# Kernel optimization log

Measured on AMD Instinct MI355X. Metric: run time of the kernel, lower is better.

Reference implementation:

```python
import jax, jax.numpy as jnp
import numpy as np

B, T, D, A = 16, 2048, 512, 64


def setup_inputs() -> dict:
    key = jax.random.key(0)
    ks = jax.random.split(key, 7)
    s = 1.0 / np.sqrt(D)
    return {
        "inp": jax.random.normal(ks[0], (B, T, D), dtype=jnp.float32),
        "Wq": jax.random.normal(ks[1], (D, A), dtype=jnp.float32) * s,
        "bq": jax.random.normal(ks[2], (A,), dtype=jnp.float32) * 0.01,
        "Wk": jax.random.normal(ks[3], (D, A), dtype=jnp.float32) * s,
        "bk": jax.random.normal(ks[4], (A,), dtype=jnp.float32) * 0.01,
        "Wv": jax.random.normal(ks[5], (D, A), dtype=jnp.float32) * s,
        "bv": jax.random.normal(ks[6], (A,), dtype=jnp.float32) * 0.01,
    }


def reference(inp, Wq, bq, Wk, bk, Wv, bv):
    # Projections: (B,T,D) @ (D,A) -> (B,T,A)
    Q = inp @ Wq + bq
    K = inp @ Wk + bk
    V = inp @ Wv + bv
    # Scaled QK^T: (B,T,T)
    scores = jnp.einsum("btd,bsd->bts", Q, K) / jnp.sqrt(jnp.float32(A))
    # Sign-based K padding mask: mask[b, s] = sign(|sum_a K[b,s,a]|)
    k_mask = jnp.sign(jnp.abs(K.sum(axis=-1)))  # (B,T)
    scores = jnp.where(k_mask[:, None, :] == 0, jnp.float32(1e-8), scores)
    att = jax.nn.softmax(scores, axis=-1)
    # Sign-based Q mask broadcast along the key axis (faithful to Mask module)
    q_mask = jnp.sign(jnp.abs(Q.sum(axis=-1)))  # (B,T)
    att = att * q_mask[:, None, :]
    # dropout_keep_prob == 1 -> dropout is identity
    ctx = jnp.einsum("bts,bsa->bta", att, V)  # (B,T,A)
    # inp^T @ ctx -> (B,D,A), then sum over A -> (B,D)
    out = jnp.einsum("btd,bta->bd", inp, ctx)
    return out
```

## Files before the change

kernel.cpp:

```cpp
#include <hip/hip_runtime.h>

#define B_ 16
#define T_ 2048
#define D_ 512
#define SCALE_LOG2E 0.18033688f

typedef __bf16 bf16x8 __attribute__((ext_vector_type(8)));
typedef float  f32x4  __attribute__((ext_vector_type(4)));

__device__ inline unsigned short f2bf(float f){
    union { float f; unsigned u; } x; x.f = f;
    unsigned r = x.u + 0x7fffu + ((x.u >> 16) & 1u);
    return (unsigned short)(r >> 16);
}

__device__ inline bf16x8 ldfrag(const unsigned short* p){
    uint4 v = *reinterpret_cast<const uint4*>(p);
    return __builtin_bit_cast(bf16x8, v);
}


__global__ void setup_kernel(const float* __restrict__ Wq, const float* __restrict__ Wk,
                             const float* __restrict__ Wv, const float* __restrict__ bq,
                             const float* __restrict__ bk, const float* __restrict__ bv,
                             unsigned short* __restrict__ WcT, float* __restrict__ bsum,
                             float* __restrict__ out)
{
    int e = blockIdx.x * 256 + threadIdx.x;
    if (e < 73728){
        int j = e >> 9, d = e & 511;
        float v;
        if (j < 64)       v = Wq[d * 64 + j];
        else if (j < 128) v = Wk[d * 64 + (j - 64)];
        else if (j < 131){
            const float* src = (j == 128) ? Wq : (j == 129) ? Wk : Wv;
            const float4* p = reinterpret_cast<const float4*>(&src[d * 64]);
            v = 0.f;
            #pragma unroll
            for (int i = 0; i < 16; i++){ float4 t = p[i]; v += (t.x + t.y) + (t.z + t.w); }
        }
        else v = 0.f;
        WcT[j * 512 + d] = f2bf(v);
    } else if (e < 73744){
        int mm = e - 73728;
        float s = 0.f;
        const float* src = (mm == 0) ? bq : (mm == 1) ? bk : bv;
        if (mm < 3){
            const float4* p = reinterpret_cast<const float4*>(src);
            #pragma unroll
            for (int i = 0; i < 16; i++){ float4 t = p[i]; s += (t.x + t.y) + (t.z + t.w); }
        }
        bsum[mm] = s;
    } else if (e < 81936){
        out[e - 73744] = 0.f;
    }
}

__global__ __launch_bounds__(256) void proj_kernel(
    const float* __restrict__ inp, const unsigned short* __restrict__ WcT,
    const float* __restrict__ bq, const float* __restrict__ bk,
    const float* __restrict__ bsum,
    unsigned short* __restrict__ Qb, unsigned short* __restrict__ Kb,
    float* __restrict__ wvp)
{
    __shared__ __align__(16) unsigned short Af[2][4 * 512];
    __shared__ __align__(16) unsigned short Bf[2][9 * 512];
    __shared__ float kzsh[64];
    const int tid  = threadIdx.x;
    const int r0   = blockIdx.x * 64;
    const int lane = tid & 63, wvid = tid >> 6;
    const int m = lane & 15, q = lane >> 4;
    const int mh = wvid >> 1, nh = wvid & 1;

    const int ar = tid >> 2, aseg = tid & 3;
    const int a_off = (ar >> 4) * 512 + (aseg * 16 + (ar & 15)) * 8;
    const float* a_src = &inp[(size_t)(r0 + ar) * 512 + aseg * 8];
    const unsigned short* b_src0 = &WcT[(((tid      ) >> 6) * 16 + (tid & 15)) * 512 + ((tid >> 4) & 3) * 8];
    const unsigned short* b_src1 = &WcT[(((tid + 256) >> 6) * 16 + (tid & 15)) * 512 + ((tid >> 4) & 3) * 8];
    const unsigned short* b_src2 = &WcT[(((tid + 512) >> 6) * 16 + (tid & 15)) * 512 + ((tid >> 4) & 3) * 8];
    const int b_off0 = tid * 8, b_off1 = (tid + 256) * 8, b_off2 = (tid + 512) * 8;

    f32x4 acc[5][2];
    #pragma unroll
    for (int t = 0; t < 5; t++){
        acc[t][0] = (f32x4){0.f, 0.f, 0.f, 0.f};
        acc[t][1] = (f32x4){0.f, 0.f, 0.f, 0.f};
    }

    float4 ga0 = *reinterpret_cast<const float4*>(a_src);
    float4 ga1 = *reinterpret_cast<const float4*>(a_src + 4);
    uint4 gb0 = *reinterpret_cast<const uint4*>(b_src0);
    uint4 gb1 = *reinterpret_cast<const uint4*>(b_src1);
    uint4 gb2 = (tid < 64) ? *reinterpret_cast<const uint4*>(b_src2) : (uint4){0,0,0,0};

    const int ntile = 5 - nh;
    const int tbase = nh * 5;

    for (int it = 0; it < 16; it++){
        const int p = it & 1;
        unsigned short* Ab = Af[p];
        unsigned short* Bb = Bf[p];
        uint4 pk;
        pk.x = f2bf(ga0.x) | ((unsigned)f2bf(ga0.y) << 16);
        pk.y = f2bf(ga0.z) | ((unsigned)f2bf(ga0.w) << 16);
        pk.z = f2bf(ga1.x) | ((unsigned)f2bf(ga1.y) << 16);
        pk.w = f2bf(ga1.z) | ((unsigned)f2bf(ga1.w) << 16);
        *reinterpret_cast<uint4*>(&Ab[a_off]) = pk;
        *reinterpret_cast<uint4*>(&Bb[b_off0]) = gb0;
        *reinterpret_cast<uint4*>(&Bb[b_off1]) = gb1;
        if (tid < 64) *reinterpret_cast<uint4*>(&Bb[b_off2]) = gb2;
        __syncthreads();
        if (it < 15){
            const int kn = (it + 1) * 32;
            ga0 = *reinterpret_cast<const float4*>(a_src + kn);
            ga1 = *reinterpret_cast<const float4*>(a_src + kn + 4);
            gb0 = *reinterpret_cast<const uint4*>(b_src0 + kn);
            gb1 = *reinterpret_cast<const uint4*>(b_src1 + kn);
            if (tid < 64) gb2 = *reinterpret_cast<const uint4*>(b_src2 + kn);
        }
        bf16x8 a0 = ldfrag(&Ab[(mh * 2    ) * 512 + lane * 8]);
        bf16x8 a1 = ldfrag(&Ab[(mh * 2 + 1) * 512 + lane * 8]);
        #pragma unroll
        for (int t = 0; t < 5; t++){
            if (t < ntile){
                bf16x8 bfr = ldfrag(&Bb[(tbase + t) * 512 + lane * 8]);
                acc[t][0] = __builtin_amdgcn_mfma_f32_16x16x32_bf16(a0, bfr, acc[t][0], 0, 0, 0);
                acc[t][1] = __builtin_amdgcn_mfma_f32_16x16x32_bf16(a1, bfr, acc[t][1], 0, 0, 0);
            }
        }
    }
    __syncthreads();

    if (nh == 1){
        const float bs = bsum[m];
        #pragma unroll
        for (int f = 0; f < 2; f++){
            #pragma unroll
            for (int i = 0; i < 4; i++){
                int rl = mh * 32 + f * 16 + q * 4 + i;
                float val = acc[3][f][i] + bs;
                float qsv = __shfl(val, (lane & 48));
                float ksv = __shfl(val, (lane & 48) | 1);
                float vsv = __shfl(val, (lane & 48) | 2);
                if (m == 0){
                    kzsh[rl] = (ksv == 0.f) ? 0.f : 1.f;
                    wvp[(size_t)r0 + rl] = (qsv == 0.f) ? 0.f : vsv;
                }
            }
        }
    }
    __syncthreads();

    if (nh == 0){
        float bqv[4];
        #pragma unroll
        for (int t = 0; t < 4; t++) bqv[t] = bq[t * 16 + m];
        const float bkv0 = bk[m];
        #pragma unroll
        for (int f = 0; f < 2; f++){
            #pragma unroll
            for (int i = 0; i < 4; i++){
                int rl = mh * 32 + f * 16 + q * 4 + i;
                size_t r = (size_t)r0 + rl;
                float kz = kzsh[rl];
                #pragma unroll
                for (int t = 0; t < 4; t++)
                    Qb[r * 64 + t * 16 + m] = f2bf((acc[t][f][i] + bqv[t]) * SCALE_LOG2E);
                Kb[r * 64 + m] = f2bf((acc[4][f][i] + bkv0) * kz);
            }
        }
    } else {
        float bkv[3];
        #pragma unroll
        for (int t = 0; t < 3; t++) bkv[t] = bk[16 + t * 16 + m];
        #pragma unroll
        for (int f = 0; f < 2; f++){
            #pragma unroll
            for (int i = 0; i < 4; i++){
                int rl = mh * 32 + f * 16 + q * 4 + i;
                size_t r = (size_t)r0 + rl;
                float kz = kzsh[rl];
                #pragma unroll
                for (int t = 0; t < 3; t++)
                    Kb[r * 64 + 16 + t * 16 + m] = f2bf((acc[t][f][i] + bkv[t]) * kz);
            }
        }
    }
}

__global__ __launch_bounds__(512) void attn_kernel(
    const unsigned short* __restrict__ Qb, const unsigned short* __restrict__ Kb,
    const float* __restrict__ wvp, float* __restrict__ num_s, float* __restrict__ den_s)
{
    __shared__ __align__(16) unsigned short Kf[2][8 * 512];
    const int tid = threadIdx.x;
    const int lane = tid & 63, wvid = tid >> 6;
    const int m = lane & 15, q = lane >> 4;
    const int b  = blockIdx.y;
    const int t0 = blockIdx.x * 256 + wvid * 32;
    const int s0 = blockIdx.z * 512;
    const size_t base = (size_t)b * T_;
    const size_t zoff = (size_t)blockIdx.z * (B_ * T_);

    const unsigned short* qp = &Qb[(base + t0 + m) * 64 + q * 8];
    bf16x8 a00 = ldfrag(qp),            a01 = ldfrag(qp + 32);
    bf16x8 a10 = ldfrag(qp + 16 * 64),  a11 = ldfrag(qp + 16 * 64 + 32);

    const unsigned short* ksrc = &Kb[(base + s0 + (wvid >> 1) * 16 + m) * 64 + (wvid & 1) * 32 + q * 8];
    const int k_off = wvid * 512 + lane * 8;
    uint4 stg = *reinterpret_cast<const uint4*>(ksrc);

    float num0[4] = {0,0,0,0}, den0[4] = {0,0,0,0};
    float num1[4] = {0,0,0,0}, den1[4] = {0,0,0,0};

    for (int it = 0; it < 8; it++){
        const int p = it & 1;
        *reinterpret_cast<uint4*>(&Kf[p][k_off]) = stg;
        __syncthreads();
        if (it < 7) stg = *reinterpret_cast<const uint4*>(ksrc + (it + 1) * 64 * 64);
        float w[4];
        #pragma unroll
        for (int st = 0; st < 4; st++) w[st] = wvp[base + s0 + it * 64 + st * 16 + m];
        #pragma unroll
        for (int st = 0; st < 4; st++){
            bf16x8 b0 = ldfrag(&Kf[p][(st * 2    ) * 512 + lane * 8]);
            bf16x8 b1 = ldfrag(&Kf[p][(st * 2 + 1) * 512 + lane * 8]);
            f32x4 z0 = (f32x4){0.f,0.f,0.f,0.f};
            z0 = __builtin_amdgcn_mfma_f32_16x16x32_bf16(a00, b0, z0, 0, 0, 0);
            z0 = __builtin_amdgcn_mfma_f32_16x16x32_bf16(a01, b1, z0, 0, 0, 0);
            f32x4 z1 = (f32x4){0.f,0.f,0.f,0.f};
            z1 = __builtin_amdgcn_mfma_f32_16x16x32_bf16(a10, b0, z1, 0, 0, 0);
            z1 = __builtin_amdgcn_mfma_f32_16x16x32_bf16(a11, b1, z1, 0, 0, 0);
            float wst = w[st];
            #pragma unroll
            for (int i = 0; i < 4; i++){
                float e0 = exp2f(z0[i]);
                den0[i] += e0; num0[i] = fmaf(e0, wst, num0[i]);
                float e1 = exp2f(z1[i]);
                den1[i] += e1; num1[i] = fmaf(e1, wst, num1[i]);
            }
        }
    }
    #pragma unroll
    for (int s = 1; s < 16; s <<= 1){
        #pragma unroll
        for (int i = 0; i < 4; i++){
            num0[i] += __shfl_xor(num0[i], s); den0[i] += __shfl_xor(den0[i], s);
            num1[i] += __shfl_xor(num1[i], s); den1[i] += __shfl_xor(den1[i], s);
        }
    }
    if (m == 0){
        #pragma unroll
        for (int i = 0; i < 4; i++){
            num_s[zoff + base + t0 + q * 4 + i]      = num0[i];
            den_s[zoff + base + t0 + q * 4 + i]      = den0[i];
            num_s[zoff + base + t0 + 16 + q * 4 + i] = num1[i];
            den_s[zoff + base + t0 + 16 + q * 4 + i] = den1[i];
        }
    }
}

__global__ __launch_bounds__(256) void out_kernel(
    const float* __restrict__ inp, const float* __restrict__ num_s,
    const float* __restrict__ den_s, float* __restrict__ out)
{
    __shared__ float csh[32];
    const int tid = threadIdx.x;
    const int b   = blockIdx.y;
    const int t0  = blockIdx.x * 32;
    const size_t base = (size_t)b * T_;
    if (tid < 32){
        size_t idx = base + t0 + tid;
        float n = num_s[idx] + num_s[32768 + idx] + num_s[65536 + idx] + num_s[98304 + idx];
        float d = den_s[idx] + den_s[32768 + idx] + den_s[65536 + idx] + den_s[98304 + idx];
        csh[tid] = n / d;
    }
    __syncthreads();
    const float2* ip = reinterpret_cast<const float2*>(inp + (base + t0) * 512);
    float a0 = 0.f, a1 = 0.f;
    #pragma unroll 8
    for (int t = 0; t < 32; t++){
        float ct = csh[t];
        float2 v = ip[(size_t)t * 256 + tid];
        a0 = fmaf(v.x, ct, a0);
        a1 = fmaf(v.y, ct, a1);
    }
    atomicAdd(&out[b * 512 + 2 * tid],     a0);
    atomicAdd(&out[b * 512 + 2 * tid + 1], a1);
}

extern "C" void kernel_launch(void* const* d_in, const int* in_sizes, int n_in,
                              void* d_out, int out_size, void* d_ws, size_t ws_size,
                              hipStream_t stream)
{
    const float* inp = (const float*)d_in[0];
    const float* Wq  = (const float*)d_in[1];
    const float* bq  = (const float*)d_in[2];
    const float* Wk  = (const float*)d_in[3];
    const float* bk  = (const float*)d_in[4];
    const float* Wv  = (const float*)d_in[5];
    const float* bv  = (const float*)d_in[6];
    float* out = (float*)d_out;

    char* ws = (char*)d_ws;
    unsigned short* WcT = (unsigned short*)(ws);
    float* bsum         = (float*)(ws + 147456);
    unsigned short* Qb  = (unsigned short*)(ws + 262144);
    unsigned short* Kb  = (unsigned short*)(ws + 4456448);
    float* wvp          = (float*)(ws + 8650752);
    float* num_s        = (float*)(ws + 8781824);
    float* den_s        = (float*)(ws + 9306112);

    setup_kernel<<<321, 256, 0, stream>>>(Wq, Wk, Wv, bq, bk, bv, WcT, bsum, out);
    proj_kernel<<<512, 256, 0, stream>>>(inp, WcT, bq, bk, bsum, Qb, Kb, wvp);
    attn_kernel<<<dim3(8, 16, 4), 512, 0, stream>>>(Qb, Kb, wvp, num_s, den_s);
    out_kernel<<<dim3(64, 16), 256, 0, stream>>>(inp, num_s, den_s, out);
}
```

Baseline: 156.7 us.

## Fuse projection, attention and output into one persistent kernel with grid barriers

```diff
diff --git a/kernel.cpp b/kernel.cpp
--- a/kernel.cpp
+++ b/kernel.cpp
@@ -3,6 +3,7 @@
 #define B_ 16
 #define T_ 2048
 #define D_ 512
+#define GRID_ 512
 #define SCALE_LOG2E 0.18033688f
 
 typedef __bf16 bf16x8 __attribute__((ext_vector_type(8)));
@@ -19,14 +20,25 @@
     return __builtin_bit_cast(bf16x8, v);
 }
 
-
-__global__ void setup_kernel(const float* __restrict__ Wq, const float* __restrict__ Wk,
-                             const float* __restrict__ Wv, const float* __restrict__ bq,
-                             const float* __restrict__ bk, const float* __restrict__ bv,
-                             unsigned short* __restrict__ WcT, float* __restrict__ bsum,
-                             float* __restrict__ out)
+__device__ inline void grid_bar(unsigned* cnt){
+    __syncthreads();
+    if (threadIdx.x == 0){
+        __hip_atomic_fetch_add(cnt, 1u, __ATOMIC_ACQ_REL, __HIP_MEMORY_SCOPE_AGENT);
+        while (__hip_atomic_load(cnt, __ATOMIC_ACQUIRE, __HIP_MEMORY_SCOPE_AGENT) < (unsigned)GRID_)
+            __builtin_amdgcn_s_sleep(1);
+    }
+    __syncthreads();
+}
+
+
+__global__ void init_kernel(const float* __restrict__ Wq, const float* __restrict__ Wk,
+                            const float* __restrict__ Wv, const float* __restrict__ bq,
+                            const float* __restrict__ bk, const float* __restrict__ bv,
+                            unsigned short* __restrict__ WcT, float* __restrict__ bsum,
+                            float* __restrict__ out, unsigned* __restrict__ bar)
 {
     int e = blockIdx.x * 256 + threadIdx.x;
+    if (e < 16) bar[e] = 0u;
     if (e < 73728){
         int j = e >> 9, d = e & 511;
         float v;
@@ -56,237 +68,250 @@
     }
 }
 
-__global__ __launch_bounds__(256) void proj_kernel(
+__global__ __launch_bounds__(256, 2) void mega_kernel(
     const float* __restrict__ inp, const unsigned short* __restrict__ WcT,
     const float* __restrict__ bq, const float* __restrict__ bk,
     const float* __restrict__ bsum,
     unsigned short* __restrict__ Qb, unsigned short* __restrict__ Kb,
-    float* __restrict__ wvp)
+    float* __restrict__ wvp, float* __restrict__ num_s, float* __restrict__ den_s,
+    float* __restrict__ out, unsigned* __restrict__ bar)
 {
-    __shared__ __align__(16) unsigned short Af[2][4 * 512];
-    __shared__ __align__(16) unsigned short Bf[2][9 * 512];
-    __shared__ float kzsh[64];
+    __shared__ union {
+        struct { __align__(16) unsigned short Af[2][2048];
+                 __align__(16) unsigned short Bf[2][4608];
+                 float kz[64]; } p;
+        struct { __align__(16) unsigned short Kf[2][4096]; } a;
+        struct { float csh[32]; } o;
+    } U;
     const int tid  = threadIdx.x;
-    const int r0   = blockIdx.x * 64;
+    const int blk  = blockIdx.x;
     const int lane = tid & 63, wvid = tid >> 6;
     const int m = lane & 15, q = lane >> 4;
-    const int mh = wvid >> 1, nh = wvid & 1;
-
-    const int ar = tid >> 2, aseg = tid & 3;
-    const int a_off = (ar >> 4) * 512 + (aseg * 16 + (ar & 15)) * 8;
-    const float* a_src = &inp[(size_t)(r0 + ar) * 512 + aseg * 8];
-    const unsigned short* b_src0 = &WcT[(((tid      ) >> 6) * 16 + (tid & 15)) * 512 + ((tid >> 4) & 3) * 8];
-    const unsigned short* b_src1 = &WcT[(((tid + 256) >> 6) * 16 + (tid & 15)) * 512 + ((tid >> 4) & 3) * 8];
-    const unsigned short* b_src2 = &WcT[(((tid + 512) >> 6) * 16 + (tid & 15)) * 512 + ((tid >> 4) & 3) * 8];
-    const int b_off0 = tid * 8, b_off1 = (tid + 256) * 8, b_off2 = (tid + 512) * 8;
-
-    f32x4 acc[5][2];
-    #pragma unroll
-    for (int t = 0; t < 5; t++){
-        acc[t][0] = (f32x4){0.f, 0.f, 0.f, 0.f};
-        acc[t][1] = (f32x4){0.f, 0.f, 0.f, 0.f};
-    }
-
-    float4 ga0 = *reinterpret_cast<const float4*>(a_src);
-    float4 ga1 = *reinterpret_cast<const float4*>(a_src + 4);
-    uint4 gb0 = *reinterpret_cast<const uint4*>(b_src0);
-    uint4 gb1 = *reinterpret_cast<const uint4*>(b_src1);
-    uint4 gb2 = (tid < 64) ? *reinterpret_cast<const uint4*>(b_src2) : (uint4){0,0,0,0};
-
-    const int ntile = 5 - nh;
-    const int tbase = nh * 5;
-
-    for (int it = 0; it < 16; it++){
-        const int p = it & 1;
-        unsigned short* Ab = Af[p];
-        unsigned short* Bb = Bf[p];
-        uint4 pk;
-        pk.x = f2bf(ga0.x) | ((unsigned)f2bf(ga0.y) << 16);
-        pk.y = f2bf(ga0.z) | ((unsigned)f2bf(ga0.w) << 16);
-        pk.z = f2bf(ga1.x) | ((unsigned)f2bf(ga1.y) << 16);
-        pk.w = f2bf(ga1.z) | ((unsigned)f2bf(ga1.w) << 16);
-        *reinterpret_cast<uint4*>(&Ab[a_off]) = pk;
-        *reinterpret_cast<uint4*>(&Bb[b_off0]) = gb0;
-        *reinterpret_cast<uint4*>(&Bb[b_off1]) = gb1;
-        if (tid < 64) *reinterpret_cast<uint4*>(&Bb[b_off2]) = gb2;
-        __syncthreads();
-        if (it < 15){
-            const int kn = (it + 1) * 32;
-            ga0 = *reinterpret_cast<const float4*>(a_src + kn);
-            ga1 = *reinterpret_cast<const float4*>(a_src + kn + 4);
-            gb0 = *reinterpret_cast<const uint4*>(b_src0 + kn);
-            gb1 = *reinterpret_cast<const uint4*>(b_src1 + kn);
-            if (tid < 64) gb2 = *reinterpret_cast<const uint4*>(b_src2 + kn);
-        }
-        bf16x8 a0 = ldfrag(&Ab[(mh * 2    ) * 512 + lane * 8]);
-        bf16x8 a1 = ldfrag(&Ab[(mh * 2 + 1) * 512 + lane * 8]);
+
+    {
+        const int r0 = blk * 64;
+        const int mh = wvid >> 1, nh = wvid & 1;
+
+        const int ar = tid >> 2, aseg = tid & 3;
+        const int a_off = (ar >> 4) * 512 + (aseg * 16 + (ar & 15)) * 8;
+        const float* a_src = &inp[(size_t)(r0 + ar) * 512 + aseg * 8];
+        const unsigned short* b_src0 = &WcT[(((tid      ) >> 6) * 16 + (tid & 15)) * 512 + ((tid >> 4) & 3) * 8];
+        const unsigned short* b_src1 = &WcT[(((tid + 256) >> 6) * 16 + (tid & 15)) * 512 + ((tid >> 4) & 3) * 8];
+        const unsigned short* b_src2 = &WcT[(((tid + 512) >> 6) * 16 + (tid & 15)) * 512 + ((tid >> 4) & 3) * 8];
+        const int b_off0 = tid * 8, b_off1 = (tid + 256) * 8, b_off2 = (tid + 512) * 8;
+
+        f32x4 acc[5][2];
         #pragma unroll
         for (int t = 0; t < 5; t++){
-            if (t < ntile){
-                bf16x8 bfr = ldfrag(&Bb[(tbase + t) * 512 + lane * 8]);
-                acc[t][0] = __builtin_amdgcn_mfma_f32_16x16x32_bf16(a0, bfr, acc[t][0], 0, 0, 0);
-                acc[t][1] = __builtin_amdgcn_mfma_f32_16x16x32_bf16(a1, bfr, acc[t][1], 0, 0, 0);
-            }
-        }
-    }
-    __syncthreads();
-
-    if (nh == 1){
-        const float bs = bsum[m];
+            acc[t][0] = (f32x4){0.f, 0.f, 0.f, 0.f};
+            acc[t][1] = (f32x4){0.f, 0.f, 0.f, 0.f};
+        }
+
+        float4 ga0 = *reinterpret_cast<const float4*>(a_src);
+        float4 ga1 = *reinterpret_cast<const float4*>(a_src + 4);
+        uint4 gb0 = *reinterpret_cast<const uint4*>(b_src0);
+        uint4 gb1 = *reinterpret_cast<const uint4*>(b_src1);
+        uint4 gb2 = (tid < 64) ? *reinterpret_cast<const uint4*>(b_src2) : (uint4){0,0,0,0};
+
+        const int ntile = 5 - nh;
+        const int tbase = nh * 5;
+
+        for (int it = 0; it < 16; it++){
+            const int p = it & 1;
+            unsigned short* Ab = U.p.Af[p];
+            unsigned short* Bb = U.p.Bf[p];
+            uint4 pk;
+            pk.x = f2bf(ga0.x) | ((unsigned)f2bf(ga0.y) << 16);
+            pk.y = f2bf(ga0.z) | ((unsigned)f2bf(ga0.w) << 16);
+            pk.z = f2bf(ga1.x) | ((unsigned)f2bf(ga1.y) << 16);
+            pk.w = f2bf(ga1.z) | ((unsigned)f2bf(ga1.w) << 16);
+            *reinterpret_cast<uint4*>(&Ab[a_off]) = pk;
+            *reinterpret_cast<uint4*>(&Bb[b_off0]) = gb0;
+            *reinterpret_cast<uint4*>(&Bb[b_off1]) = gb1;
+            if (tid < 64) *reinterpret_cast<uint4*>(&Bb[b_off2]) = gb2;
+            __syncthreads();
+            if (it < 15){
+                const int kn = (it + 1) * 32;
+                ga0 = *reinterpret_cast<const float4*>(a_src + kn);
+                ga1 = *reinterpret_cast<const float4*>(a_src + kn + 4);
+                gb0 = *reinterpret_cast<const uint4*>(b_src0 + kn);
+                gb1 = *reinterpret_cast<const uint4*>(b_src1 + kn);
+                if (tid < 64) gb2 = *reinterpret_cast<const uint4*>(b_src2 + kn);
+            }
+            bf16x8 a0 = ldfrag(&Ab[(mh * 2    ) * 512 + lane * 8]);
+            bf16x8 a1 = ldfrag(&Ab[(mh * 2 + 1) * 512 + lane * 8]);
+            #pragma unroll
+            for (int t = 0; t < 5; t++){
+                if (t < ntile){
+                    bf16x8 bfr = ldfrag(&Bb[(tbase + t) * 512 + lane * 8]);
+                    acc[t][0] = __builtin_amdgcn_mfma_f32_16x16x32_bf16(a0, bfr, acc[t][0], 0, 0, 0);
+                    acc[t][1] = __builtin_amdgcn_mfma_f32_16x16x32_bf16(a1, bfr, acc[t][1], 0, 0, 0);
+                }
+            }
+        }
+        __syncthreads();
+
+        if (nh == 1){
+            const float bs = bsum[m];
+            #pragma unroll
+            for (int f = 0; f < 2; f++){
+                #pragma unroll
+                for (int i = 0; i < 4; i++){
+                    int rl = mh * 32 + f * 16 + q * 4 + i;
+                    float val = acc[3][f][i] + bs;
+                    float qsv = __shfl(val, (lane & 48));
+                    float ksv = __shfl(val, (lane & 48) | 1);
+                    float vsv = __shfl(val, (lane & 48) | 2);
+                    if (m == 0){
+                        U.p.kz[rl] = (ksv == 0.f) ? 0.f : 1.f;
+                        wvp[(size_t)r0 + rl] = (qsv == 0.f) ? 0.f : vsv;
+                    }
+                }
+            }
+        }
+        __syncthreads();
+
+        if (nh == 0){
+            float bqv[4];
+            #pragma unroll
+            for (int t = 0; t < 4; t++) bqv[t] = bq[t * 16 + m];
+            const float bkv0 = bk[m];
+            #pragma unroll
+            for (int f = 0; f < 2; f++){
+                #pragma unroll
+                for (int i = 0; i < 4; i++){
+                    int rl = mh * 32 + f * 16 + q * 4 + i;
+                    size_t r = (size_t)r0 + rl;
+                    float kz = U.p.kz[rl];
+                    #pragma unroll
+                    for (int t = 0; t < 4; t++)
+                        Qb[r * 64 + t * 16 + m] = f2bf((acc[t][f][i] + bqv[t]) * SCALE_LOG2E);
+                    Kb[r * 64 + m] = f2bf((acc[4][f][i] + bkv0) * kz);
+                }
+            }
+        } else {
+            float bkv[3];
+            #pragma unroll
+            for (int t = 0; t < 3; t++) bkv[t] = bk[16 + t * 16 + m];
+            #pragma unroll
+            for (int f = 0; f < 2; f++){
+                #pragma unroll
+                for (int i = 0; i < 4; i++){
+                    int rl = mh * 32 + f * 16 + q * 4 + i;
+                    size_t r = (size_t)r0 + rl;
+                    float kz = U.p.kz[rl];
+                    #pragma unroll
+                    for (int t = 0; t < 3; t++)
+                        Kb[r * 64 + 16 + t * 16 + m] = f2bf((acc[t][f][i] + bkv[t]) * kz);
+                }
+            }
+        }
+    }
+
+    grid_bar(&bar[0]);
+
+    {
+        const int g  = blk * 4 + wvid;
+        const int z  = g >> 10;
+        const int bb = (g >> 6) & 15;
+        const int t0 = (g & 63) * 32;
+        const int s0 = z * 1024;
+        const size_t base = (size_t)bb * T_;
+
+        const unsigned short* qp = &Qb[(base + t0 + m) * 64 + q * 8];
+        bf16x8 a00 = ldfrag(qp),         a01 = ldfrag(qp + 32);
+        bf16x8 a10 = ldfrag(qp + 1024),  a11 = ldfrag(qp + 1024 + 32);
+
+        const unsigned short* ks0 = &Kb[(base + s0 + wvid * 16 + m) * 64 + q * 8];
+        const unsigned short* ks1 = ks0 + 32;
+        const int ko0 = (wvid * 2) * 512 + lane * 8;
+        const int ko1 = ko0 + 512;
+        uint4 st0 = *reinterpret_cast<const uint4*>(ks0);
+        uint4 st1 = *reinterpret_cast<const uint4*>(ks1);
+
+        float num0[4] = {0,0,0,0}, den0[4] = {0,0,0,0};
+        float num1[4] = {0,0,0,0}, den1[4] = {0,0,0,0};
+
+        for (int it = 0; it < 16; it++){
+            const int p = it & 1;
+            *reinterpret_cast<uint4*>(&U.a.Kf[p][ko0]) = st0;
+            *reinterpret_cast<uint4*>(&U.a.Kf[p][ko1]) = st1;
+            __syncthreads();
+            if (it < 15){
+                st0 = *reinterpret_cast<const uint4*>(ks0 + (it + 1) * 4096);
+                st1 = *reinterpret_cast<const uint4*>(ks1 + (it + 1) * 4096);
+            }
+            float w[4];
+            #pragma unroll
+            for (int st = 0; st < 4; st++) w[st] = wvp[base + s0 + it * 64 + st * 16 + m];
+            #pragma unroll
+            for (int st = 0; st < 4; st++){
+                bf16x8 b0 = ldfrag(&U.a.Kf[p][(st * 2    ) * 512 + lane * 8]);
+                bf16x8 b1 = ldfrag(&U.a.Kf[p][(st * 2 + 1) * 512 + lane * 8]);
+                f32x4 z0 = (f32x4){0.f,0.f,0.f,0.f};
+                z0 = __builtin_amdgcn_mfma_f32_16x16x32_bf16(a00, b0, z0, 0, 0, 0);
+                z0 = __builtin_amdgcn_mfma_f32_16x16x32_bf16(a01, b1, z0, 0, 0, 0);
+                f32x4 z1 = (f32x4){0.f,0.f,0.f,0.f};
+                z1 = __builtin_amdgcn_mfma_f32_16x16x32_bf16(a10, b0, z1, 0, 0, 0);
+                z1 = __builtin_amdgcn_mfma_f32_16x16x32_bf16(a11, b1, z1, 0, 0, 0);
+                float wst = w[st];
+                #pragma unroll
+                for (int i = 0; i < 4; i++){
+                    float e0 = exp2f(z0[i]);
+                    den0[i] += e0; num0[i] = fmaf(e0, wst, num0[i]);
+                    float e1 = exp2f(z1[i]);
+                    den1[i] += e1; num1[i] = fmaf(e1, wst, num1[i]);
+                }
+            }
+        }
         #pragma unroll
-        for (int f = 0; f < 2; f++){
+        for (int s = 1; s < 16; s <<= 1){
             #pragma unroll
             for (int i = 0; i < 4; i++){
-                int rl = mh * 32 + f * 16 + q * 4 + i;
-                float val = acc[3][f][i] + bs;
-                float qsv = __shfl(val, (lane & 48));
-                float ksv = __shfl(val, (lane & 48) | 1);
-                float vsv = __shfl(val, (lane & 48) | 2);
-                if (m == 0){
-                    kzsh[rl] = (ksv == 0.f) ? 0.f : 1.f;
-                    wvp[(size_t)r0 + rl] = (qsv == 0.f) ? 0.f : vsv;
-                }
-            }
-        }
-    }
-    __syncthreads();
-
-    if (nh == 0){
-        float bqv[4];
-        #pragma unroll
-        for (int t = 0; t < 4; t++) bqv[t] = bq[t * 16 + m];
-        const float bkv0 = bk[m];
-        #pragma unroll
-        for (int f = 0; f < 2; f++){
+                num0[i] += __shfl_xor(num0[i], s); den0[i] += __shfl_xor(den0[i], s);
+                num1[i] += __shfl_xor(num1[i], s); den1[i] += __shfl_xor(den1[i], s);
+            }
+        }
+        if (m == 0){
+            const size_t zo = (size_t)z * 32768;
             #pragma unroll
             for (int i = 0; i < 4; i++){
-                int rl = mh * 32 + f * 16 + q * 4 + i;
-                size_t r = (size_t)r0 + rl;
-                float kz = kzsh[rl];
-                #pragma unroll
-                for (int t = 0; t < 4; t++)
-                    Qb[r * 64 + t * 16 + m] = f2bf((acc[t][f][i] + bqv[t]) * SCALE_LOG2E);
-                Kb[r * 64 + m] = f2bf((acc[4][f][i] + bkv0) * kz);
-            }
-        }
-    } else {
-        float bkv[3];
-        #pragma unroll
-        for (int t = 0; t < 3; t++) bkv[t] = bk[16 + t * 16 + m];
-        #pragma unroll
-        for (int f = 0; f < 2; f++){
-            #pragma unroll
-            for (int i = 0; i < 4; i++){
-                int rl = mh * 32 + f * 16 + q * 4 + i;
-                size_t r = (size_t)r0 + rl;
-                float kz = kzsh[rl];
-                #pragma unroll
-                for (int t = 0; t < 3; t++)
-                    Kb[r * 64 + 16 + t * 16 + m] = f2bf((acc[t][f][i] + bkv[t]) * kz);
-            }
-        }
-    }
-}
-
-__global__ __launch_bounds__(512) void attn_kernel(
-    const unsigned short* __restrict__ Qb, const unsigned short* __restrict__ Kb,
-    const float* __restrict__ wvp, float* __restrict__ num_s, float* __restrict__ den_s)
-{
-    __shared__ __align__(16) unsigned short Kf[2][8 * 512];
-    const int tid = threadIdx.x;
-    const int lane = tid & 63, wvid = tid >> 6;
-    const int m = lane & 15, q = lane >> 4;
-    const int b  = blockIdx.y;
-    const int t0 = blockIdx.x * 256 + wvid * 32;
-    const int s0 = blockIdx.z * 512;
-    const size_t base = (size_t)b * T_;
-    const size_t zoff = (size_t)blockIdx.z * (B_ * T_);
-
-    const unsigned short* qp = &Qb[(base + t0 + m) * 64 + q * 8];
-    bf16x8 a00 = ldfrag(qp),            a01 = ldfrag(qp + 32);
-    bf16x8 a10 = ldfrag(qp + 16 * 64),  a11 = ldfrag(qp + 16 * 64 + 32);
-
-    const unsigned short* ksrc = &Kb[(base + s0 + (wvid >> 1) * 16 + m) * 64 + (wvid & 1) * 32 + q * 8];
-    const int k_off = wvid * 512 + lane * 8;
-    uint4 stg = *reinterpret_cast<const uint4*>(ksrc);
-
-    float num0[4] = {0,0,0,0}, den0[4] = {0,0,0,0};
-    float num1[4] = {0,0,0,0}, den1[4] = {0,0,0,0};
-
-    for (int it = 0; it < 8; it++){
-        const int p = it & 1;
-        *reinterpret_cast<uint4*>(&Kf[p][k_off]) = stg;
+                num_s[zo + base + t0 + q * 4 + i]      = num0[i];
+                den_s[zo + base + t0 + q * 4 + i]      = den0[i];
+                num_s[zo + base + t0 + 16 + q * 4 + i] = num1[i];
+                den_s[zo + base + t0 + 16 + q * 4 + i] = den1[i];
+            }
+        }
+    }
+
+    grid_bar(&bar[1]);
+
+    #pragma unroll
+    for (int j = 0; j < 2; j++){
+        const int tile = blk * 2 + j;
+        const int bb = tile >> 6;
+        const int t0 = (tile & 63) * 32;
+        const size_t base = (size_t)bb * T_;
         __syncthreads();
-        if (it < 7) stg = *reinterpret_cast<const uint4*>(ksrc + (it + 1) * 64 * 64);
-        float w[4];
-        #pragma unroll
-        for (int st = 0; st < 4; st++) w[st] = wvp[base + s0 + it * 64 + st * 16 + m];
-        #pragma unroll
-        for (int st = 0; st < 4; st++){
-            bf16x8 b0 = ldfrag(&Kf[p][(st * 2    ) * 512 + lane * 8]);
-            bf16x8 b1 = ldfrag(&Kf[p][(st * 2 + 1) * 512 + lane * 8]);
-            f32x4 z0 = (f32x4){0.f,0.f,0.f,0.f};
-            z0 = __builtin_amdgcn_mfma_f32_16x16x32_bf16(a00, b0, z0, 0, 0, 0);
-            z0 = __builtin_amdgcn_mfma_f32_16x16x32_bf16(a01, b1, z0, 0, 0, 0);
-            f32x4 z1 = (f32x4){0.f,0.f,0.f,0.f};
-            z1 = __builtin_amdgcn_mfma_f32_16x16x32_bf16(a10, b0, z1, 0, 0, 0);
-            z1 = __builtin_amdgcn_mfma_f32_16x16x32_bf16(a11, b1, z1, 0, 0, 0);
-            float wst = w[st];
-            #pragma unroll
-            for (int i = 0; i < 4; i++){
-                float e0 = exp2f(z0[i]);
-                den0[i] += e0; num0[i] = fmaf(e0, wst, num0[i]);
-                float e1 = exp2f(z1[i]);
-                den1[i] += e1; num1[i] = fmaf(e1, wst, num1[i]);
-            }
-        }
-    }
-    #pragma unroll
-    for (int s = 1; s < 16; s <<= 1){
-        #pragma unroll
-        for (int i = 0; i < 4; i++){
-            num0[i] += __shfl_xor(num0[i], s); den0[i] += __shfl_xor(den0[i], s);
-            num1[i] += __shfl_xor(num1[i], s); den1[i] += __shfl_xor(den1[i], s);
-        }
-    }
-    if (m == 0){
-        #pragma unroll
-        for (int i = 0; i < 4; i++){
-            num_s[zoff + base + t0 + q * 4 + i]      = num0[i];
-            den_s[zoff + base + t0 + q * 4 + i]      = den0[i];
-            num_s[zoff + base + t0 + 16 + q * 4 + i] = num1[i];
-            den_s[zoff + base + t0 + 16 + q * 4 + i] = den1[i];
-        }
-    }
-}
-
-__global__ __launch_bounds__(256) void out_kernel(
-    const float* __restrict__ inp, const float* __restrict__ num_s,
-    const float* __restrict__ den_s, float* __restrict__ out)
-{
-    __shared__ float csh[32];
-    const int tid = threadIdx.x;
-    const int b   = blockIdx.y;
-    const int t0  = blockIdx.x * 32;
-    const size_t base = (size_t)b * T_;
-    if (tid < 32){
-        size_t idx = base + t0 + tid;
-        float n = num_s[idx] + num_s[32768 + idx] + num_s[65536 + idx] + num_s[98304 + idx];
-        float d = den_s[idx] + den_s[32768 + idx] + den_s[65536 + idx] + den_s[98304 + idx];
-        csh[tid] = n / d;
-    }
-    __syncthreads();
-    const float2* ip = reinterpret_cast<const float2*>(inp + (base + t0) * 512);
-    float a0 = 0.f, a1 = 0.f;
-    #pragma unroll 8
-    for (int t = 0; t < 32; t++){
-        float ct = csh[t];
-        float2 v = ip[(size_t)t * 256 + tid];
-        a0 = fmaf(v.x, ct, a0);
-        a1 = fmaf(v.y, ct, a1);
-    }
-    atomicAdd(&out[b * 512 + 2 * tid],     a0);
-    atomicAdd(&out[b * 512 + 2 * tid + 1], a1);
+        if (tid < 32){
+            size_t idx = base + t0 + tid;
+            float n = num_s[idx] + num_s[32768 + idx];
+            float d = den_s[idx] + den_s[32768 + idx];
+            U.o.csh[tid] = n / d;
+        }
+        __syncthreads();
+        const float2* ip = reinterpret_cast<const float2*>(inp + (base + t0) * 512);
+        float a0 = 0.f, a1 = 0.f;
+        #pragma unroll 8
+        for (int t = 0; t < 32; t++){
+            float ct = U.o.csh[t];
+            float2 v = ip[(size_t)t * 256 + tid];
+            a0 = fmaf(v.x, ct, a0);
+            a1 = fmaf(v.y, ct, a1);
+        }
+        atomicAdd(&out[bb * 512 + 2 * tid],     a0);
+        atomicAdd(&out[bb * 512 + 2 * tid + 1], a1);
+    }
 }
 
 extern "C" void kernel_launch(void* const* d_in, const int* in_sizes, int n_in,
@@ -309,10 +334,10 @@
     unsigned short* Kb  = (unsigned short*)(ws + 4456448);
     float* wvp          = (float*)(ws + 8650752);
     float* num_s        = (float*)(ws + 8781824);
-    float* den_s        = (float*)(ws + 9306112);
-
-    setup_kernel<<<321, 256, 0, stream>>>(Wq, Wk, Wv, bq, bk, bv, WcT, bsum, out);
-    proj_kernel<<<512, 256, 0, stream>>>(inp, WcT, bq, bk, bsum, Qb, Kb, wvp);
-    attn_kernel<<<dim3(8, 16, 4), 512, 0, stream>>>(Qb, Kb, wvp, num_s, den_s);
-    out_kernel<<<dim3(64, 16), 256, 0, stream>>>(inp, num_s, den_s, out);
-}
+    float* den_s        = (float*)(ws + 9043968);
+    unsigned* bar       = (unsigned*)(ws + 9306112);
+
+    init_kernel<<<321, 256, 0, stream>>>(Wq, Wk, Wv, bq, bk, bv, WcT, bsum, out, bar);
+    mega_kernel<<<GRID_, 256, 0, stream>>>(inp, WcT, bq, bk, bsum, Qb, Kb, wvp,
+                                           num_s, den_s, out, bar);
+}
```

Measured after the change: 269.5 us. +71.9%, slower.
